# Kernel optimization log

Measured on AMD Instinct MI355X. Metric: run time of the kernel, lower is better.

Reference implementation:

```python
import jax, jax.numpy as jnp
import numpy as np

FEAT_STRIDE = 16
ANCHOR_SCALES = (8.0, 16.0, 32.0)
ANCHOR_RATIOS = (0.5, 1.0, 2.0)
NUM_ANCHORS = 9
PRE_NMS_TOP_N = 12000
POST_NMS_TOP_N = 300
NMS_THRESH = 0.7
POOLING_SIZE = 7
RPN_NEG_OVERLAP = 0.3
RPN_POS_OVERLAP = 0.7


def _generate_base_anchors(base_size=16):
    ratios = np.array(ANCHOR_RATIOS)
    scales = np.array(ANCHOR_SCALES)
    ctr = (base_size - 1) / 2.0
    size = float(base_size * base_size)
    ws = np.round(np.sqrt(size / ratios))
    hs = np.round(ws * ratios)
    ws = (ws[:, None] * scales[None, :]).ravel()  # order (ratio, scale)
    hs = (hs[:, None] * scales[None, :]).ravel()
    return np.stack([ctr - 0.5 * (ws - 1), ctr - 0.5 * (hs - 1),
                     ctr + 0.5 * (ws - 1), ctr + 0.5 * (hs - 1)], axis=1)


def _all_anchors(H, W):
    base = _generate_base_anchors()  # (A,4)
    sx = np.arange(W) * FEAT_STRIDE
    sy = np.arange(H) * FEAT_STRIDE
    sx, sy = np.meshgrid(sx, sy)  # (H,W)
    shifts = np.stack([sx.ravel(), sy.ravel(), sx.ravel(), sy.ravel()], axis=1)  # (H*W,4)
    anchors = (shifts[:, None, :] + base[None, :, :]).reshape(-1, 4)  # order (h,w,a)
    return jnp.asarray(anchors, dtype=jnp.float32)


def _conv(x, w, b):
    y = jax.lax.conv_general_dilated(x, w, (1, 1), 'SAME',
                                     dimension_numbers=('NCHW', 'OIHW', 'NCHW'))
    return y + b[None, :, None, None]


def _decode(anchors, deltas):
    w = anchors[:, 2] - anchors[:, 0] + 1.0
    h = anchors[:, 3] - anchors[:, 1] + 1.0
    cx = anchors[:, 0] + 0.5 * w
    cy = anchors[:, 1] + 0.5 * h
    pcx = deltas[:, 0] * w + cx
    pcy = deltas[:, 1] * h + cy
    pw = jnp.exp(deltas[:, 2]) * w
    ph = jnp.exp(deltas[:, 3]) * h
    return jnp.stack([pcx - 0.5 * pw, pcy - 0.5 * ph, pcx + 0.5 * pw, pcy + 0.5 * ph], axis=1)


def _encode(ex, gt):
    ew = ex[:, 2] - ex[:, 0] + 1.0
    eh = ex[:, 3] - ex[:, 1] + 1.0
    ecx = ex[:, 0] + 0.5 * ew
    ecy = ex[:, 1] + 0.5 * eh
    gw = gt[:, 2] - gt[:, 0] + 1.0
    gh = gt[:, 3] - gt[:, 1] + 1.0
    gcx = gt[:, 0] + 0.5 * gw
    gcy = gt[:, 1] + 0.5 * gh
    return jnp.stack([(gcx - ecx) / ew, (gcy - ecy) / eh,
                      jnp.log(gw / ew), jnp.log(gh / eh)], axis=1)


def _clip_boxes(b, im_h, im_w):
    return jnp.stack([jnp.clip(b[:, 0], 0.0, im_w - 1.0),
                      jnp.clip(b[:, 1], 0.0, im_h - 1.0),
                      jnp.clip(b[:, 2], 0.0, im_w - 1.0),
                      jnp.clip(b[:, 3], 0.0, im_h - 1.0)], axis=1)


def _iou_matrix(a, b):
    aa = (a[:, 2] - a[:, 0] + 1.0) * (a[:, 3] - a[:, 1] + 1.0)
    ba = (b[:, 2] - b[:, 0] + 1.0) * (b[:, 3] - b[:, 1] + 1.0)
    x1 = jnp.maximum(a[:, None, 0], b[None, :, 0])
    y1 = jnp.maximum(a[:, None, 1], b[None, :, 1])
    x2 = jnp.minimum(a[:, None, 2], b[None, :, 2])
    y2 = jnp.minimum(a[:, None, 3], b[None, :, 3])
    inter = jnp.maximum(x2 - x1 + 1.0, 0.0) * jnp.maximum(y2 - y1 + 1.0, 0.0)
    return inter / (aa[:, None] + ba[None, :] - inter)


def _nms(boxes, thresh, max_out):
    # boxes (N,4) already sorted by score descending; greedy NMS, fixed output size
    areas = (boxes[:, 2] - boxes[:, 0] + 1.0) * (boxes[:, 3] - boxes[:, 1] + 1.0)
    N = boxes.shape[0]

    def body(i, state):
        valid, keep = state
        idx = jnp.argmax(valid)  # first still-valid (highest score)
        has = valid[idx]
        b = boxes[idx]
        xx1 = jnp.maximum(b[0], boxes[:, 0])
        yy1 = jnp.maximum(b[1], boxes[:, 1])
        xx2 = jnp.minimum(b[2], boxes[:, 2])
        yy2 = jnp.minimum(b[3], boxes[:, 3])
        inter = jnp.maximum(xx2 - xx1 + 1.0, 0.0) * jnp.maximum(yy2 - yy1 + 1.0, 0.0)
        iou = inter / (areas[idx] + areas - inter)
        valid = jnp.where(has, valid & (iou <= thresh), valid)
        keep = keep.at[i].set(jnp.where(has, idx, 0).astype(jnp.int32))
        return valid, keep

    valid0 = jnp.ones((N,), dtype=bool)
    keep0 = jnp.zeros((max_out,), dtype=jnp.int32)
    _, keep = jax.lax.fori_loop(0, max_out, body, (valid0, keep0))
    return keep


def _roi_crop(feat, rois, P):
    # affine_grid + grid_sample (align_corners=True, zero padding), matching STRPN.pooling
    C, H, W = feat.shape[1], feat.shape[2], feat.shape[3]
    f = feat[0].reshape(C, H * W)
    R = rois.shape[0]
    x1 = rois[:, 1] / 16.0
    y1 = rois[:, 2] / 16.0
    x2 = rois[:, 3] / 16.0
    y2 = rois[:, 4] / 16.0
    t00 = (x2 - x1) / (W - 1)
    t02 = (x1 + x2 - W + 1) / (W - 1)
    t11 = (y2 - y1) / (H - 1)
    t12 = (y1 + y2 - H + 1) / (H - 1)
    lin = jnp.linspace(-1.0, 1.0, P)
    gx = jnp.broadcast_to(t00[:, None, None] * lin[None, None, :] + t02[:, None, None], (R, P, P))
    gy = jnp.broadcast_to(t11[:, None, None] * lin[None, :, None] + t12[:, None, None], (R, P, P))
    ix = (gx + 1.0) * 0.5 * (W - 1)
    iy = (gy + 1.0) * 0.5 * (H - 1)
    ix0 = jnp.floor(ix)
    iy0 = jnp.floor(iy)
    wx = ix - ix0
    wy = iy - iy0

    def gather(yi, xi, wgt):
        valid = (yi >= 0) & (yi < H) & (xi >= 0) & (xi < W)
        yc = jnp.clip(yi, 0, H - 1).astype(jnp.int32)
        xc = jnp.clip(xi, 0, W - 1).astype(jnp.int32)
        v = f[:, yc * W + xc]  # (C,R,P,P)
        return v * (wgt * valid)[None]

    out = (gather(iy0, ix0, (1 - wy) * (1 - wx)) + gather(iy0, ix0 + 1, (1 - wy) * wx)
           + gather(iy0 + 1, ix0, wy * (1 - wx)) + gather(iy0 + 1, ix0 + 1, wy * wx))
    return jnp.transpose(out, (1, 0, 2, 3))  # (R,C,P,P)


def _anchor_targets(anchors, gt_boxes, im_h, im_w):
    inside = ((anchors[:, 0] >= 0) & (anchors[:, 1] >= 0)
              & (anchors[:, 2] < im_w) & (anchors[:, 3] < im_h))
    ov = _iou_matrix(anchors, gt_boxes[:, :4])
    ov = jnp.where(inside[:, None], ov, -1.0)
    max_ov = ov.max(axis=1)
    argmax = ov.argmax(axis=1)
    gt_max = ov.max(axis=0)  # (G,)
    is_best = (ov == gt_max[None, :]).any(axis=1)
    labels = jnp.full(anchors.shape[:1], -1.0, dtype=jnp.float32)
    labels = jnp.where(inside & (max_ov < RPN_NEG_OVERLAP), 0.0, labels)
    labels = jnp.where(inside & is_best, 1.0, labels)
    labels = jnp.where(inside & (max_ov >= RPN_POS_OVERLAP), 1.0, labels)
    targets = _encode(anchors, gt_boxes[argmax, :4])
    pos = (labels == 1.0)
    ex = (labels >= 0.0)
    n_ex = jnp.maximum(ex.sum(), 1).astype(jnp.float32)
    in_w = pos[:, None].astype(jnp.float32)
    out_w = ex[:, None].astype(jnp.float32) / n_ex
    return labels, targets, in_w, out_w


def _forward(head_features, gt_boxes, im_info, rpn_w, rpn_b, cls_w, cls_b, bbox_w, bbox_b):
    A = NUM_ANCHORS
    H, W = head_features.shape[2], head_features.shape[3]
    anchors = _all_anchors(H, W)  # order (h,w,a)
    rpn = jax.nn.relu(_conv(head_features, rpn_w, rpn_b))
    cls_score = _conv(rpn, cls_w, cls_b)[0]   # (2A,H,W); channel layout cls*A + a
    bbox_pred = _conv(rpn, bbox_w, bbox_b)[0]  # (4A,H,W); channel layout a*4 + coord
    cls2 = cls_score.reshape(2, A, H, W)
    fg = jax.nn.softmax(cls2, axis=0)[1]  # (A,H,W)
    scores = jnp.transpose(fg, (1, 2, 0)).reshape(-1)  # (h,w,a)
    deltas = jnp.transpose(bbox_pred.reshape(A, 4, H, W), (2, 3, 0, 1)).reshape(-1, 4)
    im_h, im_w = im_info[0], im_info[1]
    proposals = _clip_boxes(_decode(anchors, deltas), im_h, im_w)
    _, order = jax.lax.top_k(scores, PRE_NMS_TOP_N)
    props = proposals[order]
    keep = _nms(props, NMS_THRESH, POST_NMS_TOP_N)
    sel = props[keep]
    rois = jnp.concatenate([jnp.zeros((POST_NMS_TOP_N, 1), sel.dtype), sel], axis=1)
    # RPN losses (anchor targets are numpy/constants in the original => stop_gradient)
    labels, tgt, iw, ow = jax.tree_util.tree_map(
        jax.lax.stop_gradient, _anchor_targets(anchors, gt_boxes, im_h, im_w))
    logits = jnp.transpose(cls2, (2, 3, 1, 0)).reshape(-1, 2)  # (h,w,a,2)
    logp = jax.nn.log_softmax(logits, axis=-1)
    mask = (labels >= 0).astype(logp.dtype)
    lbl = jnp.clip(labels, 0.0, 1.0).astype(jnp.int32)
    ce = -jnp.take_along_axis(logp, lbl[:, None], axis=1)[:, 0]
    cls_loss = jnp.sum(ce * mask) / jnp.maximum(mask.sum(), 1.0)
    sigma2 = 9.0  # sigma=3
    diff = iw * (deltas - tgt)
    ad = jnp.abs(diff)
    flag = (ad < 1.0 / sigma2).astype(diff.dtype)
    sl1 = flag * 0.5 * sigma2 * diff * diff + (1.0 - flag) * (ad - 0.5 / sigma2)
    box_loss = jnp.sum(ow * sl1)  # batch=1: sum over dims == mean over batch of per-image sums
    pooled = _roi_crop(head_features, jax.lax.stop_gradient(rois), POOLING_SIZE)
    return pooled, cls_loss, box_loss


def setup_inputs() -> dict:
    key = jax.random.key(0)
    ks = jax.random.split(key, 10)
    head_features = jax.random.normal(ks[0], (1, 1024, 96, 96), jnp.float32)
    G = 8
    x1 = jax.random.uniform(ks[1], (G,), minval=0.0, maxval=1100.0)
    y1 = jax.random.uniform(ks[2], (G,), minval=0.0, maxval=1000.0)
    bw = jax.random.uniform(ks[3], (G,), minval=50.0, maxval=300.0)
    bh = jax.random.uniform(ks[4], (G,), minval=100.0, maxval=450.0)
    gt_boxes = jnp.stack([x1, y1, jnp.minimum(x1 + bw, 1535.0),
                          jnp.minimum(y1 + bh, 1535.0), jnp.ones((G,))], axis=1).astype(jnp.float32)
    im_info = jnp.array([1536.0, 1536.0, 1.0], jnp.float32)
    rpn_w = jax.random.normal(ks[5], (512, 1024, 3, 3), jnp.float32) * 0.01
    rpn_b = jnp.zeros((512,), jnp.float32)
    cls_w = jax.random.normal(ks[6], (18, 512, 1, 1), jnp.float32) * 0.01
    cls_b = jnp.zeros((18,), jnp.float32)
    bbox_w = jax.random.normal(ks[7], (36, 512, 1, 1), jnp.float32) * 0.01
    bbox_b = jnp.zeros((36,), jnp.float32)
    return {"head_features": head_features, "gt_boxes": gt_boxes, "im_info": im_info,
            "rpn_w": rpn_w, "rpn_b": rpn_b, "cls_w": cls_w, "cls_b": cls_b,
            "bbox_w": bbox_w, "bbox_b": bbox_b}


def reference(head_features, gt_boxes, im_info, rpn_w, rpn_b, cls_w, cls_b, bbox_w, bbox_b):
    return _forward(head_features, gt_boxes, im_info, rpn_w, rpn_b, cls_w, cls_b, bbox_w, bbox_b)
```

## Files before the change

kernel.cpp:

```cpp
#include <hip/hip_runtime.h>
#include <stdint.h>

typedef unsigned int u32;
typedef unsigned long long u64;
typedef _Float16 f16x8 __attribute__((ext_vector_type(8)));
typedef float f32x4 __attribute__((ext_vector_type(4)));

#define HF 96
#define HW 9216
#define CIN 1024
#define CMID 512
#define NA 82944
#define PRE 12000
#define POST 300
#define NW 188
#define NBLK 324
#define OUT_POOL (POST*CIN*49)

__device__ __constant__ float BA[9][4] = {
  {-84.f,-40.f,99.f,55.f}, {-176.f,-88.f,191.f,103.f}, {-360.f,-184.f,375.f,199.f},
  {-56.f,-56.f,71.f,71.f}, {-120.f,-120.f,135.f,135.f}, {-248.f,-248.f,263.f,263.f},
  {-36.f,-80.f,51.f,95.f}, {-80.f,-168.f,95.f,183.f},  {-168.f,-344.f,183.f,359.f}
};

__device__ __forceinline__ u32 fkey(float f) {
  u32 u = __float_as_uint(f);
  return (u & 0x80000000u) ? ~u : (u | 0x80000000u);
}

__device__ __forceinline__ void gl_lds16(const void* g, void* l) {
  __builtin_amdgcn_global_load_lds((const __attribute__((address_space(1))) void*)g,
                                   (__attribute__((address_space(3))) void*)l, 16, 0, 0);
}

__global__ void prep_img(const float* __restrict__ feat, f16x8* __restrict__ img)
{
  __shared__ float ls[32][100];
  const int yy = blockIdx.x;
  const int kt = blockIdx.y;
  const int tid = threadIdx.x;
  const int y = yy - 1;
  const bool yok = (unsigned)y < 96u;
  if (yok) {
    for (int e = tid; e < 3072; e += 256) {
      const int ci = e / 96;
      const int x = e - ci * 96;
      ls[ci][x] = feat[(size_t)(kt*32 + ci)*HW + y*96 + x];
    }
  }
  __syncthreads();
  for (int idx = tid; idx < 784; idx += 256) {
    const int col = idx >> 3;
    const int q = idx & 7;
    const int x = col - 1;
    f16x8 val;
#pragma unroll
    for (int i=0;i<8;i++) val[i] = (_Float16)0.f;
    if (yok && (unsigned)x < 96u) {
#pragma unroll
      for (int i=0;i<8;i++) {
        const float v = ls[(q&3)*8 + i][x];
        if (q < 4) val[i] = (_Float16)v;
        else { const _Float16 hi = (_Float16)v; val[i] = (_Float16)((v - (float)hi)*1024.f); }
      }
    }
    const int sw = (col + 2*y) & 7;
    img[(size_t)((kt*98 + yy)*98 + col)*8 + (q ^ sw)] = val;
  }
}

__global__ void prep_w(const float* __restrict__ w, f16x8* __restrict__ wbuf)
{
  __shared__ float ls[64*289];
  const int co0 = blockIdx.x * 64;
  const int cic0 = blockIdx.y * 4;
  const int tid = threadIdx.x;
  for (int e = tid; e < 64*288; e += 256) {
    const int co = e / 288;
    const int off = e - co*288;
    ls[co*289 + off] = w[(size_t)(co0+co)*9216 + cic0*72 + off];
  }
  __syncthreads();
  const int co = tid & 63;
  for (int task = tid >> 6; task < 36; task += 4) {
    const int cic_l = task / 9;
    const int tap = task - cic_l*9;
    const int cic = cic0 + cic_l;
    const int kt = cic >> 2, kg = cic & 3;
    f16x8 hv, lv;
#pragma unroll
    for (int i=0;i<8;i++) {
      const float v = ls[co*289 + cic_l*72 + i*9 + tap] * 64.f;
      const _Float16 hi = (_Float16)v;
      hv[i] = hi;
      lv[i] = (_Float16)((v - (float)hi)*1024.f);
    }
    wbuf[(size_t)(((kt*9 + tap)*2 + 0)*4 + kg)*512 + co0 + co] = hv;
    wbuf[(size_t)(((kt*9 + tap)*2 + 1)*4 + kg)*512 + co0 + co] = lv;
  }
}

__global__ __launch_bounds__(128, 2) void rpn_conv_mfma(
    const f16x8* __restrict__ img, const f16x8* __restrict__ wbuf,
    const float* __restrict__ bias, float* __restrict__ out)
{
  __shared__ f16x8 in_s[2560];
  const int tid = threadIdx.x;
  const int lane = tid & 63;
  const int wv = tid >> 6;
  const int kgrp = lane >> 4;
  const int ln15 = lane & 15;
  const int x0 = blockIdx.x * 48;
  const int y  = blockIdx.y;
  const int co0 = blockIdx.z * 128 + wv * 64;

  int goff[10];
#pragma unroll
  for (int j=0;j<10;j++) {
    int s = j*128 + tid; if (s > 1199) s = 1199;
    const int row = s / 400;
    const int rem = s - row*400;
    goff[j] = ((y + row)*98 + x0 + (rem>>3))*8 + (rem & 7);
  }
  const int ldst0 = wv*64;

  int keyb[3];
#pragma unroll
  for (int pt=0; pt<3; ++pt) keyb[pt] = x0 + pt*16 + ln15 + 1 + 2*y;

  f32x4 acc1[4][3], acc2[4][3];
#pragma unroll
  for (int c=0;c<4;c++)
#pragma unroll
    for (int pt=0;pt<3;pt++) {
      acc1[c][pt] = (f32x4){0.f,0.f,0.f,0.f};
      acc2[c][pt] = (f32x4){0.f,0.f,0.f,0.f};
    }

  const int wlane = kgrp*512 + co0 + ln15;

#pragma unroll
  for (int j=0;j<10;j++) gl_lds16(img + goff[j], in_s + j*128 + ldst0);
  asm volatile("s_waitcnt vmcnt(0)" ::: "memory");
  __syncthreads();

  for (int kt = 0; kt < 32; ++kt) {
    const int cur = (kt & 1) * 1280;
    if (kt < 31) {
      const f16x8* kb = img + (size_t)(kt+1)*76832;
#pragma unroll
      for (int j=0;j<10;j++) gl_lds16(kb + goff[j], in_s + (1280 - cur) + j*128 + ldst0);
    }
    const f16x8* bs = in_s + cur;
#pragma unroll
    for (int t=0; t<9; ++t) {
      const int dy = t/3 - 1, dx = t%3 - 1;
      f16x8 af[4][2];
#pragma unroll
      for (int h=0;h<2;h++) {
        const size_t wb = (size_t)(((kt*9 + t)*2 + h)*2048) + wlane;
#pragma unroll
        for (int c=0;c<4;c++) af[c][h] = wbuf[wb + c*16];
      }
      f16x8 bf[3][2];
#pragma unroll
      for (int pt=0;pt<3;pt++) {
        const int key = (keyb[pt] + dx + 2*dy) & 7;
        const int base = ((dy+1)*50 + pt*16 + ln15 + dx + 1)*8;
#pragma unroll
        for (int h=0;h<2;h++)
          bf[pt][h] = bs[base + ((h*4 + kgrp) ^ key)];
      }
#pragma unroll
      for (int c=0;c<4;c++)
#pragma unroll
        for (int pt=0;pt<3;pt++) {
          acc1[c][pt] = __builtin_amdgcn_mfma_f32_16x16x32_f16(af[c][0], bf[pt][0], acc1[c][pt], 0,0,0);
          acc2[c][pt] = __builtin_amdgcn_mfma_f32_16x16x32_f16(af[c][0], bf[pt][1], acc2[c][pt], 0,0,0);
          acc2[c][pt] = __builtin_amdgcn_mfma_f32_16x16x32_f16(af[c][1], bf[pt][0], acc2[c][pt], 0,0,0);
        }
    }
    asm volatile("s_waitcnt vmcnt(0)" ::: "memory");
    __syncthreads();
  }

  const int pixb = y*96 + x0;
#pragma unroll
  for (int c=0;c<4;c++) {
#pragma unroll
    for (int i=0;i<4;i++) {
      const int co = co0 + c*16 + kgrp*4 + i;
      const float bb = bias[co];
#pragma unroll
      for (int pt=0;pt<3;pt++) {
        const float v = (acc1[c][pt][i] + acc2[c][pt][i]*(1.f/1024.f))*(1.f/64.f) + bb;
        out[(size_t)co*HW + pixb + pt*16 + ln15] = v > 0.f ? v : 0.f;
      }
    }
  }
}

__global__ void conv1x1p(const float* __restrict__ rpn,
    const float* __restrict__ cw, const float* __restrict__ bw,
    float* __restrict__ partial)
{
  const int hw = blockIdx.x * 256 + threadIdx.x;
  const int cg = blockIdx.y;
  const int ci0 = cg * 64;
  float accA[18], accB[36];
#pragma unroll
  for (int c=0;c<18;c++) accA[c]=0.f;
#pragma unroll
  for (int c=0;c<36;c++) accB[c]=0.f;
  for (int ci=ci0; ci<ci0+64; ++ci) {
    const float v = rpn[(size_t)ci*HW + hw];
#pragma unroll
    for (int c=0;c<18;c++) accA[c] = fmaf(v, cw[c*CMID+ci], accA[c]);
#pragma unroll
    for (int c=0;c<36;c++) accB[c] = fmaf(v, bw[c*CMID+ci], accB[c]);
  }
  float* p = partial + (size_t)cg*54*HW;
#pragma unroll
  for (int c=0;c<18;c++) p[(size_t)c*HW + hw] = accA[c];
#pragma unroll
  for (int c=0;c<36;c++) p[(size_t)(18+c)*HW + hw] = accB[c];
}

__global__ void conv1x1r(const float* __restrict__ partial,
    const float* __restrict__ cb, const float* __restrict__ bb,
    float* __restrict__ cls_out, float* __restrict__ bbox_out)
{
  const int o = blockIdx.x*256 + threadIdx.x;
  const int c = o / HW;
  const int hw = o - c*HW;
  float v = partial[o];
#pragma unroll
  for (int g=1; g<8; ++g) v += partial[(size_t)g*54*HW + o];
  if (c < 18) cls_out[(size_t)c*HW + hw] = v + cb[c];
  else        bbox_out[(size_t)(c-18)*HW + hw] = v + bb[c-18];
}

__global__ void score_decode_ov(const float* __restrict__ cls_out,
    const float* __restrict__ bbox_out, const float* __restrict__ im_info,
    const float* __restrict__ gt,
    u64* __restrict__ keys, float4* __restrict__ props, u32* __restrict__ hist10,
    float* __restrict__ ov, u32* __restrict__ gtmax)
{
#pragma clang fp contract(off)
  __shared__ u32 h[1024];
  __shared__ u32 lmax[8];
  const int tid = threadIdx.x;
  for (int i=tid;i<1024;i+=256) h[i]=0;
  if (tid < 8) lmax[tid] = 0u;
  __syncthreads();
  const int n = blockIdx.x*256 + tid;
  const int hw = n / 9;
  const int a  = n - hw*9;
  const int x = hw % HF, y = hw / HF;
  const float l0 = cls_out[a*HW + hw];
  const float l1 = cls_out[(9+a)*HW + hw];
  const float m = fmaxf(l0, l1);
  const float e0 = expf(l0 - m), e1 = expf(l1 - m);
  const float s = e1 / (e0 + e1);
  const u32 sb = __float_as_uint(s);
  keys[n] = ((u64)(~sb) << 32) | (u32)n;
  atomicAdd(&h[sb >> 22], 1u);

  const float ax1 = BA[a][0] + 16.f*(float)x;
  const float ay1 = BA[a][1] + 16.f*(float)y;
  const float ax2 = BA[a][2] + 16.f*(float)x;
  const float ay2 = BA[a][3] + 16.f*(float)y;
  const float aw = ax2 - ax1 + 1.f, ah = ay2 - ay1 + 1.f;
  const float cx = ax1 + 0.5f*aw,  cy = ay1 + 0.5f*ah;
  const float d0 = bbox_out[(a*4+0)*HW + hw];
  const float d1 = bbox_out[(a*4+1)*HW + hw];
  const float d2 = bbox_out[(a*4+2)*HW + hw];
  const float d3 = bbox_out[(a*4+3)*HW + hw];
  const float pcx = d0*aw + cx, pcy = d1*ah + cy;
  const float pw = expf(d2)*aw, ph = expf(d3)*ah;
  const float imh = im_info[0], imw = im_info[1];
  float bx1 = fminf(fmaxf(pcx - 0.5f*pw, 0.f), imw - 1.f);
  float by1 = fminf(fmaxf(pcy - 0.5f*ph, 0.f), imh - 1.f);
  float bx2 = fminf(fmaxf(pcx + 0.5f*pw, 0.f), imw - 1.f);
  float by2 = fminf(fmaxf(pcy + 0.5f*ph, 0.f), imh - 1.f);
  props[n] = make_float4(bx1, by1, bx2, by2);

  const bool inside = (ax1 >= 0.f) && (ay1 >= 0.f) && (ax2 < imw) && (ay2 < imh);
  const float aa = aw * ah;
#pragma unroll
  for (int j=0;j<8;j++) {
    const float g0=gt[j*5+0], g1=gt[j*5+1], g2=gt[j*5+2], g3=gt[j*5+3];
    const float ga = (g2-g0+1.f)*(g3-g1+1.f);
    const float xx1 = fmaxf(ax1,g0), yy1 = fmaxf(ay1,g1);
    const float xx2 = fminf(ax2,g2), yy2 = fminf(ay2,g3);
    const float inter = fmaxf(xx2-xx1+1.f,0.f)*fmaxf(yy2-yy1+1.f,0.f);
    const float iou = inter/(aa+ga-inter);
    const float o = inside ? iou : -1.f;
    ov[(size_t)n*8+j] = o;
    atomicMax(&lmax[j], fkey(o));
  }
  __syncthreads();
  for (int i=tid;i<1024;i+=256) if (h[i]) atomicAdd(&hist10[i], h[i]);
  if (tid < 8) atomicMax(&gtmax[tid], lmax[tid]);
}

__global__ void hist_scan1(const u32* __restrict__ hist10, u32* __restrict__ meta)
{
  __shared__ u32 c[1024];
  const int t = threadIdx.x;
  c[t] = hist10[t];
  __syncthreads();
  if (t == 0) {
    u32 cum = 0;
    int b = 1023;
    for (; b > 0; --b) {
      if (cum + c[b] >= PRE) break;
      cum += c[b];
    }
    meta[0] = (u32)b;
    meta[1] = cum;
  }
}

__global__ void refine_label(const u64* __restrict__ keys, const u32* __restrict__ meta,
                             u32* __restrict__ h64,
                             const float* __restrict__ ov, const u32* __restrict__ gtmax,
                             signed char* __restrict__ labels, signed char* __restrict__ amax,
                             int* __restrict__ exP)
{
  __shared__ u32 h[64];
  __shared__ int se[256];
  const int tid = threadIdx.x;
  if (tid < 64) h[tid] = 0;
  __syncthreads();
  const int n = blockIdx.x*256 + tid;
  const u32 sb = ~(u32)(keys[n] >> 32);
  if ((sb >> 22) == meta[0]) atomicAdd(&h[(sb >> 16) & 63], 1u);

  float best = -3.402823466e38f;
  int arg = 0;
  bool isbest = false;
#pragma unroll
  for (int j=0;j<8;j++) {
    const float o = ov[(size_t)n*8+j];
    if (o > best) { best = o; arg = j; }
    if (fkey(o) == gtmax[j]) isbest = true;
  }
  const bool inside = ov[(size_t)n*8+0] >= 0.f;
  int lab = -1;
  if (inside && best < 0.3f) lab = 0;
  if (inside && isbest) lab = 1;
  if (inside && best >= 0.7f) lab = 1;
  labels[n] = (signed char)lab;
  amax[n] = (signed char)arg;
  se[tid] = (lab >= 0) ? 1 : 0;
  __syncthreads();
  if (tid < 64 && h[tid]) atomicAdd(&h64[tid], h[tid]);
  for (int s=128; s>0; s>>=1) {
    if (tid < s) se[tid] += se[tid+s];
    __syncthreads();
  }
  if (tid==0) exP[blockIdx.x] = se[0];
}

__global__ void collect_loss(const u64* __restrict__ keys,
                             const u32* __restrict__ meta, const u32* __restrict__ h64,
                             u32* __restrict__ counter, u64* __restrict__ cand,
                             const float* __restrict__ cls_out, const float* __restrict__ bbox_out,
                             const float* __restrict__ gt, const signed char* __restrict__ labels,
                             const signed char* __restrict__ amax, float2* __restrict__ lossP)
{
#pragma clang fp contract(off)
  __shared__ float sce[256];
  __shared__ float sbx[256];
  __shared__ u32 sthr;
  const int tid = threadIdx.x;
  if (tid == 0) {
    u32 cum = meta[1];
    int s = 63;
    for (; s > 0; --s) { cum += h64[s]; if (cum >= PRE) break; }
    sthr = (meta[0] << 6) | (u32)s;
  }
  __syncthreads();
  const u32 thr = sthr;
  const int n = blockIdx.x*256 + tid;
  const u64 k = keys[n];
  const u32 sb = ~(u32)(k >> 32);
  if ((sb >> 16) >= thr) {
    u32 p = atomicAdd(counter, 1u);
    cand[p] = k;
  }
  const int hw = n/9, a = n - hw*9;
  const int lab = labels[n];
  float ce = 0.f, bx = 0.f;
  if (lab >= 0) {
    const float l0 = cls_out[a*HW+hw], l1 = cls_out[(9+a)*HW+hw];
    const float m = fmaxf(l0,l1);
    const float lse = m + logf(expf(l0-m)+expf(l1-m));
    ce = lse - (lab==1 ? l1 : l0);
  }
  if (lab == 1) {
    const int x = hw % HF, y = hw / HF;
    const float ax1 = BA[a][0]+16.f*(float)x, ay1 = BA[a][1]+16.f*(float)y;
    const float ax2 = BA[a][2]+16.f*(float)x, ay2 = BA[a][3]+16.f*(float)y;
    const float ew = ax2-ax1+1.f, eh = ay2-ay1+1.f;
    const float ecx = ax1+0.5f*ew, ecy = ay1+0.5f*eh;
    const int g = amax[n];
    const float g0=gt[g*5+0], g1=gt[g*5+1], g2=gt[g*5+2], g3=gt[g*5+3];
    const float gw = g2-g0+1.f, gh = g3-g1+1.f;
    const float gcx = g0+0.5f*gw, gcy = g1+0.5f*gh;
    float tgt[4];
    tgt[0] = (gcx-ecx)/ew;
    tgt[1] = (gcy-ecy)/eh;
    tgt[2] = logf(gw/ew);
    tgt[3] = logf(gh/eh);
#pragma unroll
    for (int j=0;j<4;j++) {
      const float d = bbox_out[(a*4+j)*HW+hw];
      const float diff = d - tgt[j];
      const float ad = fabsf(diff);
      bx += (ad < (1.0f/9.0f)) ? (4.5f*diff*diff) : (ad - 0.5f/9.0f);
    }
  }
  sce[tid]=ce; sbx[tid]=bx;
  __syncthreads();
  for (int s=128;s>0;s>>=1) {
    if (tid<s) { sce[tid]+=sce[tid+s]; sbx[tid]+=sbx[tid+s]; }
    __syncthreads();
  }
  if (tid==0) lossP[blockIdx.x] = make_float2(sce[0], sbx[0]);
}

__global__ void rank_partial(const u64* __restrict__ cand, const u32* __restrict__ counter,
                             u32* __restrict__ rankbuf)
{
  __shared__ u64 sk[256];
  const int M = (int)counter[0];
  if (blockIdx.x*256 >= M) return;
  const int i = blockIdx.x*256 + threadIdx.x;
  const u64 key = (i < M) ? cand[i] : ~0ull;
  const int chunk = ((M + 7)/8 + 255) & ~255;
  const int j0 = blockIdx.y*chunk;
  const int j1 = (j0 + chunk < M) ? (j0 + chunk) : M;
  int rank = 0;
  for (int t0 = j0; t0 < j1; t0 += 256) {
    const int j = t0 + threadIdx.x;
    sk[threadIdx.x] = (j < M) ? cand[j] : ~0ull;
    __syncthreads();
    const int lim = (j1 - t0 < 256) ? (j1 - t0) : 256;
    for (int k=0;k<lim;k++) rank += (sk[k] < key) ? 1 : 0;
    __syncthreads();
  }
  if (i < M && rank) atomicAdd(&rankbuf[i], (u32)rank);
}

__global__ void rank_scatter2(const u64* __restrict__ cand, const u32* __restrict__ counter,
                              const u32* __restrict__ rankbuf, const float4* __restrict__ props,
                              float4* __restrict__ sprops)
{
  const int M = (int)counter[0];
  const int i = blockIdx.x*256 + threadIdx.x;
  if (i >= M) return;
  const u32 r = rankbuf[i];
  if (r < PRE) sprops[r] = props[(u32)cand[i]];
}

__global__ void nms_mask(const float4* __restrict__ sp, u64* __restrict__ mask)
{
#pragma clang fp contract(off)
  const int c0 = blockIdx.x * 64;
  const int r0 = blockIdx.y * 256;
  if (c0 + 63 < r0) return;
  __shared__ float4 cb[64];
  __shared__ float  ca[64];
  const int tid = threadIdx.x;
  const int cend = min(64, PRE - c0);
  if (tid < cend) {
    float4 b = sp[c0 + tid];
    cb[tid] = b;
    ca[tid] = (b.z-b.x+1.f)*(b.w-b.y+1.f);
  }
  __syncthreads();
  const int row = r0 + tid;
  if (row >= PRE) return;
  const float4 rb = sp[row];
  const float ra = (rb.z-rb.x+1.f)*(rb.w-rb.y+1.f);
  u64 bits = 0;
  for (int j=0;j<cend;j++) {
    const float4 c = cb[j];
    const float xx1 = fmaxf(rb.x, c.x), yy1 = fmaxf(rb.y, c.y);
    const float xx2 = fminf(rb.z, c.z), yy2 = fminf(rb.w, c.w);
    const float inter = fmaxf(xx2-xx1+1.f, 0.f) * fmaxf(yy2-yy1+1.f, 0.f);
    const float iou = inter / (ra + ca[j] - inter);
    if (iou > 0.7f) bits |= (1ull << j);
  }
  mask[(size_t)row*NW + blockIdx.x] = bits;
}

__global__ void fused_scan_tr(const u64* __restrict__ mask, const float4* __restrict__ sp,
                              float* __restrict__ rois,
                              const float2* __restrict__ lossP, const int* __restrict__ exP,
                              float* __restrict__ out,
                              const float* __restrict__ feat, float* __restrict__ featT, int doT)
{
  const int b = blockIdx.x;
  if (b == 0) {
    __shared__ int keep_s[POST];
    if (threadIdx.x < 64) {
      const int l = threadIdx.x;
      u64 v[4];
#pragma unroll
      for (int q=0;q<4;q++) {
        const int w = l*4+q;
        u64 val = 0;
        if (w < NW) { val = ~0ull; if (w == NW-1) val = (1ull<<32) - 1ull; }
        v[q] = val;
      }
      for (int it=0; it<POST; ++it) {
        const u64 nz = (v[0]|v[1]) | (v[2]|v[3]);
        const u64 bal = __ballot(nz != 0);
        int idx = -1;
        if (bal != 0) {
          const int src = __ffsll((unsigned long long)bal) - 1;
          int fi = 0;
          if (v[0])      fi = (l*4+0)*64 + __ffsll(v[0]) - 1;
          else if (v[1]) fi = (l*4+1)*64 + __ffsll(v[1]) - 1;
          else if (v[2]) fi = (l*4+2)*64 + __ffsll(v[2]) - 1;
          else if (v[3]) fi = (l*4+3)*64 + __ffsll(v[3]) - 1;
          idx = __shfl(fi, src);
        }
        if (l == 0) keep_s[it] = (idx < 0) ? 0 : idx;
        if (idx >= 0 && nz != 0) {
          const u64* mrow = mask + (size_t)idx*NW + l*4;
          v[0] &= ~mrow[0]; v[1] &= ~mrow[1]; v[2] &= ~mrow[2]; v[3] &= ~mrow[3];
        }
      }
    }
    __syncthreads();
    for (int i = threadIdx.x; i < POST; i += 256) {
      const float4 bb = sp[keep_s[i]];
      rois[i*5+0] = 0.f;
      rois[i*5+1] = bb.x; rois[i*5+2] = bb.y; rois[i*5+3] = bb.z; rois[i*5+4] = bb.w;
    }
  } else if (b == 1) {
    __shared__ float a[256];
    __shared__ float c[256];
    __shared__ int   e[256];
    const int t = threadIdx.x;
    float ax = 0.f, cx = 0.f; int ev = 0;
    if (t < NBLK) { float2 v = lossP[t]; ax = v.x; cx = v.y; ev = exP[t]; }
    if (t + 256 < NBLK) { float2 v = lossP[t+256]; ax += v.x; cx += v.y; ev += exP[t+256]; }
    a[t]=ax; c[t]=cx; e[t]=ev;
    __syncthreads();
    for (int s=128;s>0;s>>=1) {
      if (t<s) { a[t]+=a[t+s]; c[t]+=c[t+s]; e[t]+=e[t+s]; }
      __syncthreads();
    }
    if (t==0) {
      const float nex = (float)max(e[0], 1);
      out[OUT_POOL+0] = a[0] / nex;
      out[OUT_POOL+1] = c[0] / nex;
    }
  } else if (doT) {
    __shared__ float t[64][65];
    const int tt = b - 2;
    const int bxhw = (tt % 144)*64, byc = (tt / 144)*64;
    const int tid = threadIdx.x;
    const int l = tid & 63, g = tid >> 6;
#pragma unroll
    for (int i=0;i<16;i++) {
      const int cL = g + 4*i;
      t[cL][l] = feat[(size_t)(byc+cL)*HW + bxhw + l];
    }
    __syncthreads();
#pragma unroll
    for (int i=0;i<16;i++) {
      const int hwL = g + 4*i;
      featT[(size_t)(bxhw+hwL)*1024 + byc + l] = t[l][hwL];
    }
  }
}

struct __align__(16) Samp { int p0,p1,p2,p3; float w0,w1,w2,w3; };

__device__ __forceinline__ Samp make_samp(const float* __restrict__ rois, int r, int s)
{
#pragma clang fp contract(off)
  const int py = s / 7, px = s - py*7;
  const float x1 = rois[r*5+1] * 0.0625f;
  const float y1 = rois[r*5+2] * 0.0625f;
  const float x2 = rois[r*5+3] * 0.0625f;
  const float y2 = rois[r*5+4] * 0.0625f;
  const float t00 = (x2-x1)/95.f;
  const float t02 = (x1+x2-95.f)/95.f;
  const float t11 = (y2-y1)/95.f;
  const float t12 = (y1+y2-95.f)/95.f;
  const float lx = (float)(px-3)/3.f;
  const float ly = (float)(py-3)/3.f;
  const float gx = t00*lx + t02;
  const float gy = t11*ly + t12;
  const float ix = (gx+1.f)*0.5f*95.f;
  const float iy = (gy+1.f)*0.5f*95.f;
  const float ix0 = floorf(ix), iy0 = floorf(iy);
  const float wx = ix-ix0, wy = iy-iy0;
  const float xs[2] = {ix0, ix0+1.f};
  const float ys[2] = {iy0, iy0+1.f};
  const float wxs[2] = {1.f-wx, wx};
  const float wys[2] = {1.f-wy, wy};
  int pos[4]; float wt[4];
#pragma unroll
  for (int k=0;k<4;k++) {
    const int dy = k>>1, dx = k&1;
    const float yi = ys[dy], xi = xs[dx];
    const bool valid = (yi>=0.f)&&(yi<96.f)&&(xi>=0.f)&&(xi<96.f);
    const int yc = (int)fminf(fmaxf(yi,0.f),95.f);
    const int xc = (int)fminf(fmaxf(xi,0.f),95.f);
    pos[k] = yc*96+xc;
    wt[k] = wys[dy]*wxs[dx] * (valid?1.f:0.f);
  }
  Samp t;
  t.p0=pos[0]; t.p1=pos[1]; t.p2=pos[2]; t.p3=pos[3];
  t.w0=wt[0];  t.w1=wt[1];  t.w2=wt[2];  t.w3=wt[3];
  return t;
}

__global__ void roi_pool_coal(const float* __restrict__ featT, const float* __restrict__ rois,
                              float* __restrict__ out)
{
#pragma clang fp contract(off)
  __shared__ float st[49][257];
  __shared__ Samp sam[49];
  const int tid = threadIdx.x;
  const int r = blockIdx.x, cb = blockIdx.y;
  if (tid < 49) sam[tid] = make_samp(rois, r, tid);
  __syncthreads();
  const int c = cb*256 + tid;
  for (int s=0;s<49;s++) {
    const Samp t = sam[s];
    st[s][tid] = t.w0*featT[(size_t)t.p0*1024+c] + t.w1*featT[(size_t)t.p1*1024+c]
               + t.w2*featT[(size_t)t.p2*1024+c] + t.w3*featT[(size_t)t.p3*1024+c];
  }
  __syncthreads();
  float* ob = out + (size_t)r*50176 + cb*12544;
  for (int i=tid; i<12544; i+=256) {
    const int cL = i / 49, s = i - cL*49;
    ob[i] = st[s][cL];
  }
}

__global__ void roi_pool_gather(const float* __restrict__ feat, const float* __restrict__ rois,
                                float* __restrict__ out)
{
#pragma clang fp contract(off)
  const int o = blockIdx.x*256 + threadIdx.x;
  const int s  = o % 49;
  const int rc = o / 49;
  const int c = rc & (CIN-1);
  const int r = rc >> 10;
  const Samp t = make_samp(rois, r, s);
  const float* f = feat + (size_t)c*HW;
  out[o] = t.w0*f[t.p0] + t.w1*f[t.p1] + t.w2*f[t.p2] + t.w3*f[t.p3];
}

extern "C" void kernel_launch(void* const* d_in, const int* in_sizes, int n_in,
                              void* d_out, int out_size, void* d_ws, size_t ws_size,
                              hipStream_t stream)
{
  const float* feat    = (const float*)d_in[0];
  const float* gt      = (const float*)d_in[1];
  const float* im_info = (const float*)d_in[2];
  const float* rpn_w   = (const float*)d_in[3];
  const float* rpn_b   = (const float*)d_in[4];
  const float* cls_w   = (const float*)d_in[5];
  const float* cls_b   = (const float*)d_in[6];
  const float* bbox_w  = (const float*)d_in[7];
  const float* bbox_b  = (const float*)d_in[8];
  float* out = (float*)d_out;
  char* ws = (char*)d_ws;

  size_t off = 0;
  auto alloc = [&](size_t bytes) {
    size_t o = off;
    off = (off + bytes + 255) & ~(size_t)255;
    return o;
  };
  size_t o_counter = alloc(4);
  size_t o_gtmax   = alloc(32);
  size_t o_meta    = alloc(8);
  size_t o_h64     = alloc(256);
  size_t o_hist10  = alloc(1024*4);
  size_t o_rank    = alloc((size_t)NA*4);
  size_t zeroBytes = off;
  size_t o_cls  = alloc((size_t)18*HW*4);
  size_t o_bbox = alloc((size_t)36*HW*4);
  size_t o_rpn  = alloc((size_t)CMID*HW*4);
  size_t o_R = off;
  const size_t IMG_BYTES  = (size_t)32*98*98*8*16;
  const size_t WBUF_BYTES = (size_t)9*2*128*512*16;
  const size_t FEATT_BYTES= (size_t)HW*1024*4;
  size_t o_img  = o_R;
  size_t o_wbuf = o_R + ((IMG_BYTES + 255) & ~(size_t)255);
  size_t baseC_A = o_R + ((FEATT_BYTES + 255) & ~(size_t)255);
  auto phaseC = [&](size_t base, size_t* offs) {
    size_t co = base;
    auto ca = [&](size_t bytes) { size_t o = co; co = (co + bytes + 255) & ~(size_t)255; return o; };
    offs[0] = ca((size_t)8*54*HW*4);
    co = base;
    offs[1] = ca((size_t)NA*8);
    offs[2] = ca((size_t)NA*16);
    offs[3] = ca((size_t)NA*8);
    offs[4] = ca((size_t)PRE*16);
    offs[5] = ca((size_t)PRE*NW*8);
    offs[6] = ca((size_t)POST*5*4);
    offs[7] = ca((size_t)NA*8*4);
    offs[8] = ca((size_t)NA);
    offs[9] = ca((size_t)NA);
    offs[10]= ca((size_t)NBLK*4);
    offs[11]= ca((size_t)NBLK*8);
    size_t endC = co;
    size_t endB = base + (size_t)8*54*HW*4;
    return endC > endB ? endC : endB;
  };
  size_t offsA[12], offsB[12];
  size_t endA = phaseC(baseC_A, offsA);
  size_t convEnd = o_wbuf + WBUF_BYTES;
  size_t neededA = (endA > convEnd ? endA : convEnd);
  size_t endB = phaseC(o_R, offsB);
  (void)endB;
  const bool useT = (ws_size >= neededA);
  const size_t* offs = useT ? offsA : offsB;
  (void)in_sizes; (void)n_in; (void)out_size;

  hipMemsetAsync(ws, 0, zeroBytes, stream);

  f16x8* img      = (f16x8*)(ws + o_img);
  f16x8* wbuf     = (f16x8*)(ws + o_wbuf);
  float* featT    = (float*)(ws + o_R);
  float* partial  = (float*)(ws + offs[0]);
  float* rpn      = (float*)(ws + o_rpn);
  float* cls_out  = (float*)(ws + o_cls);
  float* bbox_out = (float*)(ws + o_bbox);
  u64*   keys     = (u64*)(ws + offs[1]);
  float4* props   = (float4*)(ws + offs[2]);
  u64*   cand     = (u64*)(ws + offs[3]);
  float4* sprops  = (float4*)(ws + offs[4]);
  u64*   maskp    = (u64*)(ws + offs[5]);
  float* rois     = (float*)(ws + offs[6]);
  float* ovp      = (float*)(ws + offs[7]);
  signed char* labels = (signed char*)(ws + offs[8]);
  signed char* amax   = (signed char*)(ws + offs[9]);
  int*    exP     = (int*)(ws + offs[10]);
  float2* lossP   = (float2*)(ws + offs[11]);
  u32* counter    = (u32*)(ws + o_counter);
  u32* gtmaxp     = (u32*)(ws + o_gtmax);
  u32* metap      = (u32*)(ws + o_meta);
  u32* h64p       = (u32*)(ws + o_h64);
  u32* hist10     = (u32*)(ws + o_hist10);
  u32* rankbuf    = (u32*)(ws + o_rank);

  prep_img<<<dim3(98,32), 256, 0, stream>>>(feat, img);
  prep_w<<<dim3(8,32), 256, 0, stream>>>(rpn_w, wbuf);
  rpn_conv_mfma<<<dim3(2,96,4), 128, 0, stream>>>(img, wbuf, rpn_b, rpn);
  conv1x1p<<<dim3(36,8), 256, 0, stream>>>(rpn, cls_w, bbox_w, partial);
  conv1x1r<<<54*HW/256, 256, 0, stream>>>(partial, cls_b, bbox_b, cls_out, bbox_out);
  score_decode_ov<<<NBLK, 256, 0, stream>>>(cls_out, bbox_out, im_info, gt,
                                            keys, props, hist10, ovp, gtmaxp);
  hist_scan1<<<1, 1024, 0, stream>>>(hist10, metap);
  refine_label<<<NBLK, 256, 0, stream>>>(keys, metap, h64p, ovp, gtmaxp, labels, amax, exP);
  collect_loss<<<NBLK, 256, 0, stream>>>(keys, metap, h64p, counter, cand,
                                         cls_out, bbox_out, gt, labels, amax, lossP);
  rank_partial<<<dim3(NBLK,8), 256, 0, stream>>>(cand, counter, rankbuf);
  rank_scatter2<<<NBLK, 256, 0, stream>>>(cand, counter, rankbuf, props, sprops);
  nms_mask<<<dim3(NW, 47), 256, 0, stream>>>(sprops, maskp);
  fused_scan_tr<<<2306, 256, 0, stream>>>(maskp, sprops, rois, lossP, exP, out,
                                          feat, featT, useT ? 1 : 0);
  if (useT) roi_pool_coal<<<dim3(POST,4), 256, 0, stream>>>(featT, rois, out);
  else      roi_pool_gather<<<OUT_POOL/256, 256, 0, stream>>>(feat, rois, out);
}
```

Before: 700.4 us.

## Retile RPN 3x3 conv to two output rows per block with narrower channel slices

Each conv block now covers two output rows by 48 pixels and 64 output channels, instead of one row by 48 pixels and 128 channels. Each wave handles 32 channels across 6 pixel tiles rather than 64 channels across 3. This trades more reuse of the staged input halo (4 rows staged for 2 output rows, up from 3 for 1) against more weight reloads across blocks. The grid becomes a 1D launch of 768 blocks with the 8 channel groups innermost, so neighbouring blocks share input rows in cache. LDS use per block rises to hold the larger input tile.

New measurement: 954.4 us. 36.3% more time.

```diff
diff --git a/kernel.cpp b/kernel.cpp
--- a/kernel.cpp
+++ b/kernel.cpp
@@ -104,35 +104,39 @@
     const f16x8* __restrict__ img, const f16x8* __restrict__ wbuf,
     const float* __restrict__ bias, float* __restrict__ out)
 {
-  __shared__ f16x8 in_s[2560];
+  __shared__ f16x8 in_s[3328];
+  const int bid = blockIdx.x;
+  const int cg  = bid & 7;
+  const int seq = bid >> 3;
+  const int x0 = (seq & 1) * 48;
+  const int y0 = (seq >> 1) * 2;
   const int tid = threadIdx.x;
   const int lane = tid & 63;
   const int wv = tid >> 6;
   const int kgrp = lane >> 4;
   const int ln15 = lane & 15;
-  const int x0 = blockIdx.x * 48;
-  const int y  = blockIdx.y;
-  const int co0 = blockIdx.z * 128 + wv * 64;
-
-  int goff[10];
-#pragma unroll
-  for (int j=0;j<10;j++) {
-    int s = j*128 + tid; if (s > 1199) s = 1199;
+  const int co0 = cg*64 + wv*32;
+
+  int goff[13];
+#pragma unroll
+  for (int j=0;j<13;j++) {
+    int s = j*128 + tid; if (s > 1599) s = 1599;
     const int row = s / 400;
     const int rem = s - row*400;
-    goff[j] = ((y + row)*98 + x0 + (rem>>3))*8 + (rem & 7);
+    goff[j] = ((y0 + row)*98 + x0 + (rem>>3))*8 + (rem & 7);
   }
   const int ldst0 = wv*64;
 
-  int keyb[3];
-#pragma unroll
-  for (int pt=0; pt<3; ++pt) keyb[pt] = x0 + pt*16 + ln15 + 1 + 2*y;
-
-  f32x4 acc1[4][3], acc2[4][3];
-#pragma unroll
-  for (int c=0;c<4;c++)
-#pragma unroll
-    for (int pt=0;pt<3;pt++) {
+  int keyb[6];
+#pragma unroll
+  for (int pt=0; pt<6; ++pt)
+    keyb[pt] = x0 + (pt%3)*16 + ln15 + 1 + 2*(y0 + pt/3);
+
+  f32x4 acc1[2][6], acc2[2][6];
+#pragma unroll
+  for (int c=0;c<2;c++)
+#pragma unroll
+    for (int pt=0;pt<6;pt++) {
       acc1[c][pt] = (f32x4){0.f,0.f,0.f,0.f};
       acc2[c][pt] = (f32x4){0.f,0.f,0.f,0.f};
     }
@@ -140,61 +144,66 @@
   const int wlane = kgrp*512 + co0 + ln15;
 
 #pragma unroll
-  for (int j=0;j<10;j++) gl_lds16(img + goff[j], in_s + j*128 + ldst0);
+  for (int j=0;j<13;j++) gl_lds16(img + goff[j], in_s + j*128 + ldst0);
   asm volatile("s_waitcnt vmcnt(0)" ::: "memory");
   __syncthreads();
 
   for (int kt = 0; kt < 32; ++kt) {
-    const int cur = (kt & 1) * 1280;
+    const int cur = (kt & 1) * 1664;
     if (kt < 31) {
       const f16x8* kb = img + (size_t)(kt+1)*76832;
 #pragma unroll
-      for (int j=0;j<10;j++) gl_lds16(kb + goff[j], in_s + (1280 - cur) + j*128 + ldst0);
+      for (int j=0;j<13;j++) gl_lds16(kb + goff[j], in_s + (1664 - cur) + j*128 + ldst0);
     }
     const f16x8* bs = in_s + cur;
 #pragma unroll
     for (int t=0; t<9; ++t) {
       const int dy = t/3 - 1, dx = t%3 - 1;
-      f16x8 af[4][2];
+      f16x8 af[2][2];
 #pragma unroll
       for (int h=0;h<2;h++) {
         const size_t wb = (size_t)(((kt*9 + t)*2 + h)*2048) + wlane;
 #pragma unroll
-        for (int c=0;c<4;c++) af[c][h] = wbuf[wb + c*16];
+        for (int c=0;c<2;c++) af[c][h] = wbuf[wb + c*16];
       }
-      f16x8 bf[3][2];
-#pragma unroll
-      for (int pt=0;pt<3;pt++) {
-        const int key = (keyb[pt] + dx + 2*dy) & 7;
-        const int base = ((dy+1)*50 + pt*16 + ln15 + dx + 1)*8;
-#pragma unroll
-        for (int h=0;h<2;h++)
-          bf[pt][h] = bs[base + ((h*4 + kgrp) ^ key)];
+#pragma unroll
+      for (int half=0; half<2; ++half) {
+        const int rowL = half + dy + 1;
+        f16x8 bf[3][2];
+#pragma unroll
+        for (int p3=0;p3<3;p3++) {
+          const int pt = half*3 + p3;
+          const int key = (keyb[pt] + dx + 2*dy) & 7;
+          const int base = (rowL*50 + p3*16 + ln15 + dx + 1)*8;
+#pragma unroll
+          for (int h=0;h<2;h++)
+            bf[p3][h] = bs[base + ((h*4 + kgrp) ^ key)];
+        }
+#pragma unroll
+        for (int c=0;c<2;c++)
+#pragma unroll
+          for (int p3=0;p3<3;p3++) {
+            const int pt = half*3 + p3;
+            acc1[c][pt] = __builtin_amdgcn_mfma_f32_16x16x32_f16(af[c][0], bf[p3][0], acc1[c][pt], 0,0,0);
+            acc2[c][pt] = __builtin_amdgcn_mfma_f32_16x16x32_f16(af[c][0], bf[p3][1], acc2[c][pt], 0,0,0);
+            acc2[c][pt] = __builtin_amdgcn_mfma_f32_16x16x32_f16(af[c][1], bf[p3][0], acc2[c][pt], 0,0,0);
+          }
       }
-#pragma unroll
-      for (int c=0;c<4;c++)
-#pragma unroll
-        for (int pt=0;pt<3;pt++) {
-          acc1[c][pt] = __builtin_amdgcn_mfma_f32_16x16x32_f16(af[c][0], bf[pt][0], acc1[c][pt], 0,0,0);
-          acc2[c][pt] = __builtin_amdgcn_mfma_f32_16x16x32_f16(af[c][0], bf[pt][1], acc2[c][pt], 0,0,0);
-          acc2[c][pt] = __builtin_amdgcn_mfma_f32_16x16x32_f16(af[c][1], bf[pt][0], acc2[c][pt], 0,0,0);
-        }
     }
     asm volatile("s_waitcnt vmcnt(0)" ::: "memory");
     __syncthreads();
   }
 
-  const int pixb = y*96 + x0;
-#pragma unroll
-  for (int c=0;c<4;c++) {
+#pragma unroll
+  for (int c=0;c<2;c++) {
 #pragma unroll
     for (int i=0;i<4;i++) {
       const int co = co0 + c*16 + kgrp*4 + i;
       const float bb = bias[co];
 #pragma unroll
-      for (int pt=0;pt<3;pt++) {
+      for (int pt=0;pt<6;pt++) {
         const float v = (acc1[c][pt][i] + acc2[c][pt][i]*(1.f/1024.f))*(1.f/64.f) + bb;
-        out[(size_t)co*HW + pixb + pt*16 + ln15] = v > 0.f ? v : 0.f;
+        out[(size_t)co*HW + (y0 + pt/3)*96 + x0 + (pt%3)*16 + ln15] = v > 0.f ? v : 0.f;
       }
     }
   }
@@ -760,7 +769,7 @@
 
   prep_img<<<dim3(98,32), 256, 0, stream>>>(feat, img);
   prep_w<<<dim3(8,32), 256, 0, stream>>>(rpn_w, wbuf);
-  rpn_conv_mfma<<<dim3(2,96,4), 128, 0, stream>>>(img, wbuf, rpn_b, rpn);
+  rpn_conv_mfma<<<768, 128, 0, stream>>>(img, wbuf, rpn_b, rpn);
   conv1x1p<<<dim3(36,8), 256, 0, stream>>>(rpn, cls_w, bbox_w, partial);
   conv1x1r<<<54*HW/256, 256, 0, stream>>>(partial, cls_b, bbox_b, cls_out, bbox_out);
   score_decode_ov<<<NBLK, 256, 0, stream>>>(cls_out, bbox_out, im_info, gt,
```

## Chunk NMS scan into 512-box slices staged in shared memory

Applied to the files above, without the earlier changes.

Replaces the serial 300-iteration NMS scan, where each step waited on a dependent global load of a full mask row, with a chunked scan. Each chunk of 512 candidates first has its suppression bits cleared in parallel by earlier kept boxes using shared-memory atomics. It then stages the chunk's mask slice in LDS and runs the greedy selection from shared memory. This takes global-memory latency off the serial critical path, at the cost of extra parallel loads, atomics and block-wide syncs per chunk.

New measurement: 607.7 us (median of 2 runs). -13.2%, faster.

```diff
diff --git a/kernel.cpp b/kernel.cpp
--- a/kernel.cpp
+++ b/kernel.cpp
@@ -505,39 +505,61 @@
 {
   const int b = blockIdx.x;
   if (b == 0) {
+    __shared__ u64 mslice[4096];
+    __shared__ u64 vbits[8];
     __shared__ int keep_s[POST];
-    if (threadIdx.x < 64) {
-      const int l = threadIdx.x;
-      u64 v[4];
-#pragma unroll
-      for (int q=0;q<4;q++) {
-        const int w = l*4+q;
-        u64 val = 0;
-        if (w < NW) { val = ~0ull; if (w == NW-1) val = (1ull<<32) - 1ull; }
-        v[q] = val;
+    __shared__ int s_nsel;
+    const int tid = threadIdx.x;
+    for (int i = tid; i < POST; i += 256) keep_s[i] = 0;
+    if (tid == 0) s_nsel = 0;
+    __syncthreads();
+    for (int c = 0; c < 24; ++c) {
+      if (s_nsel >= POST) break;
+      const int base = c * 512;
+      const int cnt = (PRE - base < 512) ? (PRE - base) : 512;
+      if (tid < 8) {
+        u64 v = 0;
+        const int lo = tid * 64;
+        if (lo < cnt) {
+          v = ~0ull;
+          const int rem = cnt - lo;
+          if (rem < 64) v = (1ull << rem) - 1ull;
+        }
+        vbits[tid] = v;
       }
-      for (int it=0; it<POST; ++it) {
-        const u64 nz = (v[0]|v[1]) | (v[2]|v[3]);
-        const u64 bal = __ballot(nz != 0);
-        int idx = -1;
-        if (bal != 0) {
+      __syncthreads();
+      for (int k = tid; k < cnt*8; k += 256) {
+        const int i = k >> 3, w = k & 7;
+        mslice[k] = mask[(size_t)(base + i)*NW + c*8 + w];
+      }
+      const int ns = s_nsel;
+      for (int k = tid; k < ns*8; k += 256) {
+        const int s = k >> 3, w = k & 7;
+        const u64 row = mask[(size_t)keep_s[s]*NW + c*8 + w];
+        if (row) atomicAnd(&vbits[w], ~row);
+      }
+      __syncthreads();
+      if (tid < 64) {
+        const int l = tid;
+        u64 v = (l < 8) ? vbits[l] : 0;
+        int nsel = s_nsel;
+        for (;;) {
+          const u64 bal = __ballot(v != 0);
+          if (bal == 0) break;
           const int src = __ffsll((unsigned long long)bal) - 1;
           int fi = 0;
-          if (v[0])      fi = (l*4+0)*64 + __ffsll(v[0]) - 1;
-          else if (v[1]) fi = (l*4+1)*64 + __ffsll(v[1]) - 1;
-          else if (v[2]) fi = (l*4+2)*64 + __ffsll(v[2]) - 1;
-          else if (v[3]) fi = (l*4+3)*64 + __ffsll(v[3]) - 1;
-          idx = __shfl(fi, src);
+          if (v) fi = l*64 + __ffsll(v) - 1;
+          const int il = __shfl(fi, src);
+          if (l == 0) keep_s[nsel] = base + il;
+          nsel++;
+          if (nsel >= POST) break;
+          if (l < 8) v &= ~mslice[(il << 3) | l];
         }
-        if (l == 0) keep_s[it] = (idx < 0) ? 0 : idx;
-        if (idx >= 0 && nz != 0) {
-          const u64* mrow = mask + (size_t)idx*NW + l*4;
-          v[0] &= ~mrow[0]; v[1] &= ~mrow[1]; v[2] &= ~mrow[2]; v[3] &= ~mrow[3];
-        }
+        if (l == 0) s_nsel = nsel;
       }
-    }
-    __syncthreads();
-    for (int i = threadIdx.x; i < POST; i += 256) {
+      __syncthreads();
+    }
+    for (int i = tid; i < POST; i += 256) {
       const float4 bb = sp[keep_s[i]];
       rois[i*5+0] = 0.f;
       rois[i*5+1] = bb.x; rois[i*5+2] = bb.y; rois[i*5+3] = bb.z; rois[i*5+4] = bb.w;
```
